# Performance work log

Hardware: AMD Instinct MI355X
Metric: run time of the kernel (lower is better)

The kernel has to match this reference:

```python
import jax, jax.numpy as jnp
import numpy as np

NP, NA = 200000, 100000        # paper / author node counts
EW, EC = 300000, 300000        # writes / cites edge counts
HID, H, D = 128, 4, 32         # hidden, heads, head dim
FIN_P, FIN_A, OUT = 256, 128, 16
SCALE = float(1.0 / np.sqrt(D))


def _seg_softmax(alpha, idx, n):
    # softmax over edges grouped by destination node (PyG softmax)
    m = jax.ops.segment_max(alpha, idx, num_segments=n)
    e = jnp.exp(alpha - m[idx])
    s = jax.ops.segment_sum(e, idx, num_segments=n)
    return e / (s[idx] + 1e-16)


def _edge_type(k_src, v_src, q_dst, src, dst, a_rel, m_rel, p_rel, n_dst):
    # per-relation transform at node level, then gather-attend-scatter
    kr = jnp.einsum('nhd,hde->nhe', k_src, a_rel)
    vr = jnp.einsum('nhd,hde->nhe', v_src, m_rel)
    alpha = jnp.sum(q_dst[dst] * kr[src], axis=-1) * p_rel * SCALE  # [E,H]
    alpha = _seg_softmax(alpha, dst, n_dst)
    return jax.ops.segment_sum(vr[src] * alpha[..., None], dst, num_segments=n_dst)


def setup_inputs() -> dict:
    key = jax.random.key(0)
    ks = iter(jax.random.split(key, 48))

    def nrm(shape, s=0.05):
        return jax.random.normal(next(ks), shape, jnp.float32) * s

    inp = dict(
        x_paper=nrm((NP, FIN_P), 1.0),
        x_author=nrm((NA, FIN_A), 1.0),
        writes_src=jax.random.randint(next(ks), (EW,), 0, NA, dtype=jnp.int32),
        writes_dst=jax.random.randint(next(ks), (EW,), 0, NP, dtype=jnp.int32),
        cites_src=jax.random.randint(next(ks), (EC,), 0, NP, dtype=jnp.int32),
        cites_dst=jax.random.randint(next(ks), (EC,), 0, NP, dtype=jnp.int32),
        lin_paper_w=nrm((FIN_P, HID)), lin_paper_b=jnp.zeros((HID,), jnp.float32),
        lin_author_w=nrm((FIN_A, HID)), lin_author_b=jnp.zeros((HID,), jnp.float32),
        lin_out_w=nrm((HID, OUT)), lin_out_b=jnp.zeros((OUT,), jnp.float32),
    )
    for t in ('paper', 'author'):
        for nm in ('k', 'q', 'v', 'a'):
            inp[f'{nm}_w_{t}'] = nrm((HID, HID))
            inp[f'{nm}_b_{t}'] = jnp.zeros((HID,), jnp.float32)
        inp[f'skip_{t}'] = jnp.ones((), jnp.float32)
    for e in ('writes', 'cites'):
        inp[f'a_rel_{e}'] = nrm((H, D, D), 0.18)
        inp[f'm_rel_{e}'] = nrm((H, D, D), 0.18)
        inp[f'p_rel_{e}'] = jnp.ones((H,), jnp.float32)
    return inp


def reference(x_paper, x_author, writes_src, writes_dst, cites_src, cites_dst,
              lin_paper_w, lin_paper_b, lin_author_w, lin_author_b,
              lin_out_w, lin_out_b,
              k_w_paper, k_b_paper, q_w_paper, q_b_paper, v_w_paper, v_b_paper,
              a_w_paper, a_b_paper, skip_paper,
              k_w_author, k_b_author, q_w_author, q_b_author, v_w_author, v_b_author,
              a_w_author, a_b_author, skip_author,
              a_rel_writes, m_rel_writes, p_rel_writes,
              a_rel_cites, m_rel_cites, p_rel_cites):
    # per-node-type input projection + relu
    hp = jax.nn.relu(x_paper @ lin_paper_w + lin_paper_b)
    ha = jax.nn.relu(x_author @ lin_author_w + lin_author_b)
    # HGTConv: per-node-type k/q/v, [N,H,D]
    k_p = (hp @ k_w_paper + k_b_paper).reshape(NP, H, D)
    q_p = (hp @ q_w_paper + q_b_paper).reshape(NP, H, D)
    v_p = (hp @ v_w_paper + v_b_paper).reshape(NP, H, D)
    k_a = (ha @ k_w_author + k_b_author).reshape(NA, H, D)
    v_a = (ha @ v_w_author + v_b_author).reshape(NA, H, D)
    # heterogeneous multi-relation attention, group='sum' over edge types
    out_p = _edge_type(k_a, v_a, q_p, writes_src, writes_dst,
                       a_rel_writes, m_rel_writes, p_rel_writes, NP)
    out_p = out_p + _edge_type(k_p, v_p, q_p, cites_src, cites_dst,
                               a_rel_cites, m_rel_cites, p_rel_cites, NP)
    # output projection + gated skip (paper type; only 'paper' feeds the head)
    op = jax.nn.gelu(out_p.reshape(NP, HID), approximate=False) @ a_w_paper + a_b_paper
    beta = jax.nn.sigmoid(skip_paper)
    hp = beta * op + (1.0 - beta) * hp
    return hp @ lin_out_w + lin_out_b  # [NP, OUT]
```

## Files before the change

kernel.cpp:

```cpp
#include <hip/hip_runtime.h>
#include <cstdint>

#define NP 200000
#define NA 100000
#define EW 300000
#define EC 300000
#define HID 128
#define FIN_P 256
#define FIN_A 128
#define NOUT 16
#define ATT_SCALE 0.17677669529663687f

#define NBP 1563
#define NBA 782

#define SCAN_N (2 * NP)
#define SCAN_BS 256
#define SCAN_ITEMS 4
#define SCAN_TILE 1024
#define SCAN_NB ((SCAN_N + SCAN_TILE - 1) / SCAN_TILE)

typedef short s8v __attribute__((ext_vector_type(8)));
typedef float f32x4 __attribute__((ext_vector_type(4)));
typedef unsigned short ushort_t;

__device__ __forceinline__ float gelu_f(float x) {
  return 0.5f * x * (1.0f + erff(x * 0.70710678118654752f));
}
__device__ __forceinline__ ushort_t f2bf(float f) {
  unsigned u = __float_as_uint(f);
  return (ushort_t)((u + 0x7FFFu + ((u >> 16) & 1u)) >> 16);
}
__device__ __forceinline__ unsigned pack2bf(float a, float b) {
  return (unsigned)f2bf(a) | ((unsigned)f2bf(b) << 16);
}
__device__ __forceinline__ unsigned cvtpk(float a, float b) {
  unsigned r;
  asm("v_cvt_pk_bf16_f32 %0, %1, %2" : "=v"(r) : "v"(a), "v"(b));
  return r;
}
__device__ __forceinline__ float bflo(unsigned u) { return __uint_as_float(u << 16); }
__device__ __forceinline__ float bfhi(unsigned u) { return __uint_as_float(u & 0xFFFF0000u); }

__device__ __forceinline__ void gl16(const void* g, void* l) {
  __builtin_amdgcn_global_load_lds(
      (const __attribute__((address_space(1))) void*)g,
      (__attribute__((address_space(3))) void*)l, 16, 0, 0);
}

__device__ __forceinline__ int s2row(int r) { return (r ^ (r >> 2)) & 3; }

__global__ void prep_all(
    const float* __restrict__ qw,  const float* __restrict__ qb,
    const float* __restrict__ kwp, const float* __restrict__ kbp, const float* __restrict__ arc,
    const float* __restrict__ vwp, const float* __restrict__ vbp, const float* __restrict__ mrc,
    const float* __restrict__ kwa, const float* __restrict__ kba, const float* __restrict__ arw,
    const float* __restrict__ vwa, const float* __restrict__ vba, const float* __restrict__ mrw,
    const float* __restrict__ lpw, const float* __restrict__ law,
    const float* __restrict__ aw, const float* __restrict__ ab,
    const float* __restrict__ skip, const float* __restrict__ W2, const float* __restrict__ b2,
    ushort_t* __restrict__ Wall, float* __restrict__ Ball,
    float* __restrict__ Wg, float* __restrict__ Wh, float* __restrict__ bo,
    int* __restrict__ cnt)
{
  const int b = blockIdx.x, tid = threadIdx.x;
  if (b == 0) {
    for (int idx = tid; idx < 16384; idx += 256) {
      int c = idx >> 7, r = idx & 127;
      Wall[idx] = f2bf(qw[r * 128 + c]);
    }
    for (int c = tid; c < 128; c += 256) Ball[c] = qb[c];
  } else if (b <= 4) {
    const float *W, *bias, *rel;
    switch (b) {
      case 1:  W = kwp; bias = kbp; rel = arc; break;
      case 2:  W = vwp; bias = vbp; rel = mrc; break;
      case 3:  W = kwa; bias = kba; rel = arw; break;
      default: W = vwa; bias = vba; rel = mrw; break;
    }
    for (int idx = tid; idx < 16384; idx += 256) {
      int c = idx >> 7, r = idx & 127, h = c >> 5, e = c & 31;
      float s = 0.f;
      #pragma unroll
      for (int d = 0; d < 32; ++d) s += W[r * 128 + h * 32 + d] * rel[h * 1024 + d * 32 + e];
      Wall[b * 16384 + idx] = f2bf(s);
    }
    for (int c = tid; c < 128; c += 256) {
      int h = c >> 5, e = c & 31;
      float s = 0.f;
      #pragma unroll
      for (int d = 0; d < 32; ++d) s += bias[h * 32 + d] * rel[h * 1024 + d * 32 + e];
      Ball[b * 128 + c] = s;
    }
  } else if (b == 5) {
    for (int idx = tid; idx < 16384; idx += 256) {
      int c = idx >> 7, r = idx & 127;
      Wall[5 * 16384 + idx] = f2bf(law[r * 128 + c]);
    }
  } else if (b == 6) {
    for (int idx = tid; idx < 32768; idx += 256) {
      int c = idx >> 8, r = idx & 255;
      Wall[6 * 16384 + idx] = f2bf(lpw[r * 128 + c]);
    }
  } else if (b == 7) {
    float beta = 1.0f / (1.0f + expf(-skip[0]));
    for (int idx = tid; idx < 128 * 16; idx += 256) {
      int r = idx >> 4, c = idx & 15;
      float s = 0.f;
      for (int k = 0; k < 128; ++k) s += aw[r * 128 + k] * W2[k * 16 + c];
      Wg[idx] = beta * s;
      Wh[idx] = (1.0f - beta) * W2[idx];
    }
    if (tid < 16) {
      float s = 0.f;
      for (int k = 0; k < 128; ++k) s += ab[k] * W2[k * 16 + tid];
      bo[tid] = beta * s + b2[tid];
    }
  } else {
    int chunk = SCAN_N / 8;
    int base = (b - 8) * chunk;
    for (int i = tid; i < chunk; i += 256) cnt[base + i] = 0;
  }
}

__global__ __launch_bounds__(256) void gemm_proj(
    const float* __restrict__ xp, const float* __restrict__ xa,
    const ushort_t* __restrict__ Wall,
    const float* __restrict__ bp, const float* __restrict__ ba,
    ushort_t* __restrict__ hpo, ushort_t* __restrict__ hao)
{
  __shared__ ushort_t As[4096];
  __shared__ ushort_t Bs[4096];
  const bool isP = blockIdx.x < NBP;
  const int bid = isP ? blockIdx.x : blockIdx.x - NBP;
  const float* A = isP ? xp : xa;
  const ushort_t* W = Wall + (isP ? 6 * 16384 : 5 * 16384);
  const float* bias = isP ? bp : ba;
  ushort_t* C = isP ? hpo : hao;
  const int M = isP ? NP : NA;
  const int KT = isP ? 256 : 128;
  const int nt = KT >> 5;

  const int tid  = threadIdx.x;
  const int lane = tid & 63;
  const int wv   = tid >> 6;
  const int wr   = wv >> 1, wc = wv & 1;
  const int l15  = lane & 15, kgl = lane >> 4;
  const int s2l  = (l15 ^ (l15 >> 2)) & 3;
  const int row0 = bid * 128;

  const int r0 = tid >> 2, kgp = tid & 3;
  const int sk = kgp ^ s2row(r0);
  int g0 = row0 + r0;       if (g0 > M - 1) g0 = M - 1;
  int g1 = row0 + r0 + 64;  if (g1 > M - 1) g1 = M - 1;
  const float* a0p = A + (size_t)g0 * KT + sk * 8;
  const float* a1p = A + (size_t)g1 * KT + sk * 8;
  const ushort_t* b0p = W + (size_t)r0 * KT + sk * 8;
  const ushort_t* b1p = W + (size_t)(r0 + 64) * KT + sk * 8;
  ushort_t* asd0 = &As[(size_t)tid * 8];
  ushort_t* asd1 = &As[(size_t)(tid + 256) * 8];

  f32x4 acc[4][4];
  #pragma unroll
  for (int i = 0; i < 4; ++i)
    #pragma unroll
    for (int j = 0; j < 4; ++j) acc[i][j] = (f32x4){0.f, 0.f, 0.f, 0.f};

  for (int kt = 0; kt < KT; kt += 32) {
    gl16(b0p + kt, &Bs[(size_t)tid * 8]);
    gl16(b1p + kt, &Bs[(size_t)(tid + 256) * 8]);
    float4 fa0 = *(const float4*)(a0p + kt);
    float4 fa1 = *(const float4*)(a0p + kt + 4);
    float4 fa2 = *(const float4*)(a1p + kt);
    float4 fa3 = *(const float4*)(a1p + kt + 4);
    uint4 v0, v1;
    v0.x = cvtpk(fa0.x, fa0.y); v0.y = cvtpk(fa0.z, fa0.w);
    v0.z = cvtpk(fa1.x, fa1.y); v0.w = cvtpk(fa1.z, fa1.w);
    v1.x = cvtpk(fa2.x, fa2.y); v1.y = cvtpk(fa2.z, fa2.w);
    v1.z = cvtpk(fa3.x, fa3.y); v1.w = cvtpk(fa3.z, fa3.w);
    *(uint4*)asd0 = v0;
    *(uint4*)asd1 = v1;
    __syncthreads();

    const s8v* As8 = (const s8v*)As;
    const s8v* Bs8 = (const s8v*)Bs;
    s8v af[4], bfv[4];
    #pragma unroll
    for (int i = 0; i < 4; ++i)
      af[i]  = As8[(wr * 64 + i * 16 + l15) * 4 + (kgl ^ s2l)];
    #pragma unroll
    for (int j = 0; j < 4; ++j)
      bfv[j] = Bs8[(wc * 64 + j * 16 + l15) * 4 + (kgl ^ s2l)];
    #pragma unroll
    for (int i = 0; i < 4; ++i)
      #pragma unroll
      for (int j = 0; j < 4; ++j)
        acc[i][j] = __builtin_amdgcn_mfma_f32_16x16x32_bf16(af[i], bfv[j], acc[i][j], 0, 0, 0);
    __syncthreads();
  }

  float bv[4];
  #pragma unroll
  for (int j = 0; j < 4; ++j) bv[j] = bias[wc * 64 + j * 16 + l15];
  #pragma unroll
  for (int i = 0; i < 4; ++i) {
    #pragma unroll
    for (int r = 0; r < 4; ++r) {
      int row = row0 + wr * 64 + i * 16 + kgl * 4 + r;
      if (row < M) {
        #pragma unroll
        for (int j = 0; j < 4; ++j) {
          float v = acc[i][j][r] + bv[j];
          v = fmaxf(v, 0.f);
          C[(size_t)row * 128 + wc * 64 + j * 16 + l15] = f2bf(v);
        }
      }
    }
  }
}

__global__ __launch_bounds__(256) void gemm_kv(
    const ushort_t* __restrict__ hpA, const ushort_t* __restrict__ haA,
    const ushort_t* __restrict__ Wall, const float* __restrict__ Ball,
    ushort_t* __restrict__ qkv, ushort_t* __restrict__ kvw)
{
  __shared__ ushort_t As[4096];
  __shared__ ushort_t Bs[4096];
  int b = blockIdx.x;
  int set, bid, M;
  const ushort_t* A;
  ushort_t* C;
  if (b < 3 * NBP) {
    set = b / NBP; bid = b - set * NBP;
    A = hpA; M = NP;
    C = qkv + (size_t)set * NP * HID;
  } else {
    int t = b - 3 * NBP;
    int s2 = t / NBA; bid = t - s2 * NBA;
    set = 3 + s2;
    A = haA; M = NA;
    C = kvw + (size_t)s2 * NA * HID;
  }
  const ushort_t* W = Wall + set * 16384;
  const float* bias = Ball + set * 128;

  const int tid  = threadIdx.x;
  const int lane = tid & 63;
  const int wv   = tid >> 6;
  const int wr   = wv >> 1, wc = wv & 1;
  const int l15  = lane & 15, kgl = lane >> 4;
  const int s2l  = (l15 ^ (l15 >> 2)) & 3;
  const int row0 = bid * 128;

  const int r0 = tid >> 2, kgp = tid & 3;
  const int sk = kgp ^ s2row(r0);
  int g0 = row0 + r0;       if (g0 > M - 1) g0 = M - 1;
  int g1 = row0 + r0 + 64;  if (g1 > M - 1) g1 = M - 1;
  const ushort_t* a0p = A + (size_t)g0 * 128 + sk * 8;
  const ushort_t* a1p = A + (size_t)g1 * 128 + sk * 8;
  const ushort_t* b0p = W + (size_t)r0 * 128 + sk * 8;
  const ushort_t* b1p = W + (size_t)(r0 + 64) * 128 + sk * 8;

  f32x4 acc[4][4];
  #pragma unroll
  for (int i = 0; i < 4; ++i)
    #pragma unroll
    for (int j = 0; j < 4; ++j) acc[i][j] = (f32x4){0.f, 0.f, 0.f, 0.f};

  #pragma unroll
  for (int t = 0; t < 4; ++t) {
    int kt = t * 32;
    gl16(a0p + kt, &As[(size_t)tid * 8]);
    gl16(a1p + kt, &As[(size_t)(tid + 256) * 8]);
    gl16(b0p + kt, &Bs[(size_t)tid * 8]);
    gl16(b1p + kt, &Bs[(size_t)(tid + 256) * 8]);
    __syncthreads();

    const s8v* As8 = (const s8v*)As;
    const s8v* Bs8 = (const s8v*)Bs;
    s8v af[4], bfv[4];
    #pragma unroll
    for (int i = 0; i < 4; ++i)
      af[i]  = As8[(wr * 64 + i * 16 + l15) * 4 + (kgl ^ s2l)];
    #pragma unroll
    for (int j = 0; j < 4; ++j)
      bfv[j] = Bs8[(wc * 64 + j * 16 + l15) * 4 + (kgl ^ s2l)];
    #pragma unroll
    for (int i = 0; i < 4; ++i)
      #pragma unroll
      for (int j = 0; j < 4; ++j)
        acc[i][j] = __builtin_amdgcn_mfma_f32_16x16x32_bf16(af[i], bfv[j], acc[i][j], 0, 0, 0);
    __syncthreads();
  }

  float bv[4];
  #pragma unroll
  for (int j = 0; j < 4; ++j) bv[j] = bias[wc * 64 + j * 16 + l15];
  #pragma unroll
  for (int i = 0; i < 4; ++i) {
    #pragma unroll
    for (int r = 0; r < 4; ++r) {
      int row = row0 + wr * 64 + i * 16 + kgl * 4 + r;
      if (row < M) {
        #pragma unroll
        for (int j = 0; j < 4; ++j) {
          C[(size_t)row * 128 + wc * 64 + j * 16 + l15] = f2bf(acc[i][j][r] + bv[j]);
        }
      }
    }
  }
}

__global__ void hist_k(const int* __restrict__ wdst, const int* __restrict__ cdst,
                       int* __restrict__ cnt)
{
  int t = blockIdx.x * blockDim.x + threadIdx.x;
  if (t < EW) atomicAdd(&cnt[wdst[t]], 1);
  if (t < EC) atomicAdd(&cnt[NP + cdst[t]], 1);
}

__global__ __launch_bounds__(SCAN_BS) void scan1(const int* __restrict__ cnt,
                                                 int* __restrict__ off,
                                                 int* __restrict__ bsum)
{
  __shared__ int sh[2][SCAN_BS];
  int tid = threadIdx.x;
  int base = blockIdx.x * SCAN_TILE + tid * SCAN_ITEMS;
  int v[SCAN_ITEMS]; int tsum = 0;
  #pragma unroll
  for (int i = 0; i < SCAN_ITEMS; ++i) {
    int idx = base + i;
    v[i] = (idx < SCAN_N) ? cnt[idx] : 0;
    tsum += v[i];
  }
  int p = 0;
  sh[0][tid] = tsum; __syncthreads();
  #pragma unroll
  for (int d = 1; d < SCAN_BS; d <<= 1) {
    int x = sh[p][tid] + ((tid >= d) ? sh[p][tid - d] : 0);
    sh[p ^ 1][tid] = x; __syncthreads(); p ^= 1;
  }
  int run = sh[p][tid] - tsum;
  #pragma unroll
  for (int i = 0; i < SCAN_ITEMS; ++i) {
    int idx = base + i;
    if (idx < SCAN_N) off[idx] = run;
    run += v[i];
  }
  if (tid == SCAN_BS - 1) bsum[blockIdx.x] = sh[p][tid];
}

__global__ __launch_bounds__(512) void scan2(int* __restrict__ bsum)
{
  __shared__ int sh[2][512];
  int tid = threadIdx.x;
  int v = (tid < SCAN_NB) ? bsum[tid] : 0;
  int p = 0;
  sh[0][tid] = v; __syncthreads();
  for (int d = 1; d < 512; d <<= 1) {
    int x = sh[p][tid] + ((tid >= d) ? sh[p][tid - d] : 0);
    sh[p ^ 1][tid] = x; __syncthreads(); p ^= 1;
  }
  if (tid < SCAN_NB) bsum[tid] = sh[p][tid] - v;
}

__global__ __launch_bounds__(SCAN_BS) void scan3(int* __restrict__ off, int* __restrict__ cur,
                                                 const int* __restrict__ bsum)
{
  int add = bsum[blockIdx.x];
  int base = blockIdx.x * SCAN_TILE + threadIdx.x;
  #pragma unroll
  for (int i = 0; i < SCAN_ITEMS; ++i) {
    int idx = base + i * SCAN_BS;
    if (idx < SCAN_N) { int t = off[idx] + add; off[idx] = t; cur[idx] = t; }
  }
  if (blockIdx.x == 0 && threadIdx.x == 0) off[SCAN_N] = EW + EC;
}

__global__ void fill_k(const int* __restrict__ wsrc, const int* __restrict__ wdst,
                       const int* __restrict__ csrc, const int* __restrict__ cdst,
                       int* __restrict__ cur, int* __restrict__ esrc)
{
  int t = blockIdx.x * blockDim.x + threadIdx.x;
  if (t < EW) { int p = atomicAdd(&cur[wdst[t]], 1); esrc[p] = wsrc[t] << 8; }
  if (t < EC) { int p = atomicAdd(&cur[NP + cdst[t]], 1); esrc[p] = csrc[t] << 8; }
}

__global__ __launch_bounds__(256) void node_attn(
    const int* __restrict__ off, const int* __restrict__ esrc,
    const ushort_t* __restrict__ q,
    const ushort_t* __restrict__ kr_w, const ushort_t* __restrict__ vr_w,
    const ushort_t* __restrict__ kr_c, const ushort_t* __restrict__ vr_c,
    const float* __restrict__ p_rel_w, const float* __restrict__ p_rel_c,
    ushort_t* __restrict__ out_p)
{
  int gid = blockIdx.x * blockDim.x + threadIdx.x;
  int node = gid >> 4;
  int l16 = gid & 15;
  int h = l16 >> 2;

  uint4 qv = *(const uint4*)(q + (size_t)node * HID + l16 * 8);
  float qf[8];
  {
    const unsigned* pq = (const unsigned*)&qv;
    #pragma unroll
    for (int w = 0; w < 4; ++w) { qf[2 * w] = bflo(pq[w]); qf[2 * w + 1] = bfhi(pq[w]); }
  }
  float prw = p_rel_w[h] * ATT_SCALE;
  float prc = p_rel_c[h] * ATT_SCALE;
  unsigned loff = (unsigned)(l16 * 16);

  float t[8];
  #pragma unroll
  for (int i = 0; i < 8; ++i) t[i] = 0.f;

  #pragma unroll
  for (int r = 0; r < 2; ++r) {
    const char* krb = (const char*)((r == 0) ? kr_w : kr_c);
    const char* vrb = (const char*)((r == 0) ? vr_w : vr_c);
    float prr = (r == 0) ? prw : prc;
    int eb = off[(r == 0 ? 0 : NP) + node];
    int ee = off[(r == 0 ? 0 : NP) + node + 1];

    float s = 0.f;
    float A[8];
    #pragma unroll
    for (int i = 0; i < 8; ++i) A[i] = 0.f;

    for (int e = eb; e < ee; ++e) {
      unsigned kb = (unsigned)esrc[e] + loff;
      uint4 kv = *(const uint4*)(krb + kb);
      uint4 vv = *(const uint4*)(vrb + kb);
      const unsigned* pk = (const unsigned*)&kv;
      float d = 0.f;
      #pragma unroll
      for (int w = 0; w < 4; ++w) {
        d = fmaf(qf[2 * w], bflo(pk[w]), d);
        d = fmaf(qf[2 * w + 1], bfhi(pk[w]), d);
      }
      d += __shfl_xor(d, 1);
      d += __shfl_xor(d, 2);
      float p = __expf(d * prr);
      s += p;
      const unsigned* pv = (const unsigned*)&vv;
      #pragma unroll
      for (int w = 0; w < 4; ++w) {
        A[2 * w]     = fmaf(p, bflo(pv[w]), A[2 * w]);
        A[2 * w + 1] = fmaf(p, bfhi(pv[w]), A[2 * w + 1]);
      }
    }
    float inv = 1.0f / (s + 1e-16f);
    #pragma unroll
    for (int i = 0; i < 8; ++i) t[i] = fmaf(A[i], inv, t[i]);
  }

  uint4 o;
  unsigned* po = (unsigned*)&o;
  #pragma unroll
  for (int w = 0; w < 4; ++w) po[w] = pack2bf(t[2 * w], t[2 * w + 1]);
  *(uint4*)(out_p + (size_t)node * HID + l16 * 8) = o;
}

__global__ __launch_bounds__(256) void epilogue_k(
    const ushort_t* __restrict__ out_p, const ushort_t* __restrict__ hp,
    const float* __restrict__ Wg, const float* __restrict__ Wh,
    const float* __restrict__ bo, float* __restrict__ out)
{
  __shared__ float Ts[64][129];
  __shared__ float Wgs[128][16];
  __shared__ float Whs[128][16];
  __shared__ float bs[16];
  int tid = threadIdx.x;
  int row0 = blockIdx.x * 64;

  #pragma unroll
  for (int i = 0; i < 2; ++i) {
    int idx = tid + i * 256;
    *(float4*)&Wgs[idx >> 2][(idx & 3) << 2] = *(const float4*)(Wg + (size_t)idx * 4);
    *(float4*)&Whs[idx >> 2][(idx & 3) << 2] = *(const float4*)(Wh + (size_t)idx * 4);
  }
  if (tid < 16) bs[tid] = bo[tid];

  #pragma unroll
  for (int i = 0; i < 4; ++i) {
    int idx = tid + i * 256;
    int r = idx >> 4, c8 = (idx & 15) << 3;
    uint4 g = *(const uint4*)(out_p + (size_t)(row0 + r) * HID + c8);
    const unsigned* pw = (const unsigned*)&g;
    #pragma unroll
    for (int w = 0; w < 4; ++w) {
      Ts[r][c8 + 2 * w]     = gelu_f(bflo(pw[w]));
      Ts[r][c8 + 2 * w + 1] = gelu_f(bfhi(pw[w]));
    }
  }
  __syncthreads();

  int row = tid & 63, cg = tid >> 6;
  float acc[4];
  #pragma unroll
  for (int j = 0; j < 4; ++j) acc[j] = bs[cg * 4 + j];
  for (int k = 0; k < 128; ++k) {
    float g = Ts[row][k];
    float4 w = *(const float4*)&Wgs[k][cg << 2];
    acc[0] = fmaf(g, w.x, acc[0]); acc[1] = fmaf(g, w.y, acc[1]);
    acc[2] = fmaf(g, w.z, acc[2]); acc[3] = fmaf(g, w.w, acc[3]);
  }
  __syncthreads();

  #pragma unroll
  for (int i = 0; i < 4; ++i) {
    int idx = tid + i * 256;
    int r = idx >> 4, c8 = (idx & 15) << 3;
    uint4 hh = *(const uint4*)(hp + (size_t)(row0 + r) * HID + c8);
    const unsigned* pw = (const unsigned*)&hh;
    #pragma unroll
    for (int w = 0; w < 4; ++w) {
      Ts[r][c8 + 2 * w]     = bflo(pw[w]);
      Ts[r][c8 + 2 * w + 1] = bfhi(pw[w]);
    }
  }
  __syncthreads();
  for (int k = 0; k < 128; ++k) {
    float hv = Ts[row][k];
    float4 w = *(const float4*)&Whs[k][cg << 2];
    acc[0] = fmaf(hv, w.x, acc[0]); acc[1] = fmaf(hv, w.y, acc[1]);
    acc[2] = fmaf(hv, w.z, acc[2]); acc[3] = fmaf(hv, w.w, acc[3]);
  }
  *(float4*)(out + (size_t)(row0 + row) * NOUT + (cg << 2)) =
      make_float4(acc[0], acc[1], acc[2], acc[3]);
}

extern "C" void kernel_launch(void* const* d_in, const int* in_sizes, int n_in,
                              void* d_out, int out_size, void* d_ws, size_t ws_size,
                              hipStream_t stream)
{
  (void)in_sizes; (void)n_in; (void)out_size; (void)ws_size;
  const float* x_paper      = (const float*)d_in[0];
  const float* x_author     = (const float*)d_in[1];
  const int*   writes_src   = (const int*)d_in[2];
  const int*   writes_dst   = (const int*)d_in[3];
  const int*   cites_src    = (const int*)d_in[4];
  const int*   cites_dst    = (const int*)d_in[5];
  const float* lin_paper_w  = (const float*)d_in[6];
  const float* lin_paper_b  = (const float*)d_in[7];
  const float* lin_author_w = (const float*)d_in[8];
  const float* lin_author_b = (const float*)d_in[9];
  const float* lin_out_w    = (const float*)d_in[10];
  const float* lin_out_b    = (const float*)d_in[11];
  const float* k_w_paper    = (const float*)d_in[12];
  const float* k_b_paper    = (const float*)d_in[13];
  const float* q_w_paper    = (const float*)d_in[14];
  const float* q_b_paper    = (const float*)d_in[15];
  const float* v_w_paper    = (const float*)d_in[16];
  const float* v_b_paper    = (const float*)d_in[17];
  const float* a_w_paper    = (const float*)d_in[18];
  const float* a_b_paper    = (const float*)d_in[19];
  const float* skip_paper   = (const float*)d_in[20];
  const float* k_w_author   = (const float*)d_in[21];
  const float* k_b_author   = (const float*)d_in[22];
  const float* v_w_author   = (const float*)d_in[25];
  const float* v_b_author   = (const float*)d_in[26];
  const float* a_rel_writes = (const float*)d_in[30];
  const float* m_rel_writes = (const float*)d_in[31];
  const float* p_rel_writes = (const float*)d_in[32];
  const float* a_rel_cites  = (const float*)d_in[33];
  const float* m_rel_cites  = (const float*)d_in[34];
  const float* p_rel_cites  = (const float*)d_in[35];

  float* ws = (float*)d_ws;
  size_t off_f = 0;
  auto nxt = [&](size_t nfloats) { float* p = ws + off_f; off_f += nfloats; return p; };
  ushort_t* hp    = (ushort_t*)nxt((size_t)NP * 64);
  ushort_t* ha    = (ushort_t*)nxt((size_t)NA * 64);
  ushort_t* qkv   = (ushort_t*)nxt((size_t)3 * NP * 64);
  ushort_t* kvw   = (ushort_t*)nxt((size_t)2 * NA * 64);
  ushort_t* outp  = (ushort_t*)nxt((size_t)NP * 64);
  int*      cnt   = (int*)nxt(SCAN_N);
  int*      offs  = (int*)nxt(SCAN_N + 2);
  int*      cur   = (int*)nxt(SCAN_N);
  int*      esrc  = (int*)nxt(EW + EC);
  int*      bsum  = (int*)nxt(512);
  ushort_t* Wall  = (ushort_t*)nxt(65536);
  float*    Ball  = nxt(5 * 128);
  float*    Wg    = nxt(2048);
  float*    Wh    = nxt(2048);
  float*    bo    = nxt(16);

  ushort_t* q_p  = qkv;
  ushort_t* kr_c = qkv + (size_t)NP * HID;
  ushort_t* vr_c = qkv + (size_t)2 * NP * HID;
  ushort_t* kr_w = kvw;
  ushort_t* vr_w = kvw + (size_t)NA * HID;

  prep_all<<<16, 256, 0, stream>>>(q_w_paper, q_b_paper,
                                   k_w_paper, k_b_paper, a_rel_cites,
                                   v_w_paper, v_b_paper, m_rel_cites,
                                   k_w_author, k_b_author, a_rel_writes,
                                   v_w_author, v_b_author, m_rel_writes,
                                   lin_paper_w, lin_author_w,
                                   a_w_paper, a_b_paper, skip_paper, lin_out_w, lin_out_b,
                                   Wall, Ball, Wg, Wh, bo, cnt);

  hist_k<<<(300000 + 255) / 256, 256, 0, stream>>>(writes_dst, cites_dst, cnt);
  scan1<<<SCAN_NB, SCAN_BS, 0, stream>>>(cnt, offs, bsum);
  scan2<<<1, 512, 0, stream>>>(bsum);
  scan3<<<SCAN_NB, SCAN_BS, 0, stream>>>(offs, cur, bsum);
  fill_k<<<(300000 + 255) / 256, 256, 0, stream>>>(writes_src, writes_dst,
                                                   cites_src, cites_dst, cur, esrc);

  gemm_proj<<<NBP + NBA, 256, 0, stream>>>(x_paper, x_author, Wall,
                                           lin_paper_b, lin_author_b, hp, ha);
  gemm_kv<<<3 * NBP + 2 * NBA, 256, 0, stream>>>(hp, ha, Wall, Ball, qkv, kvw);

  node_attn<<<(NP * 16) / 256, 256, 0, stream>>>(
      offs, esrc, q_p, kr_w, vr_w, kr_c, vr_c, p_rel_writes, p_rel_cites, outp);

  epilogue_k<<<(NP + 63) / 64, 256, 0, stream>>>(outp, hp, Wg, Wh, bo, (float*)d_out);
}
```

Before: 439.7 us.

## Reuse A tile across all weight sets in gemm_kv and prefetch first edges in attention

New measurement: 425.3 us. 3.3% less time.

```diff
diff --git a/kernel.cpp b/kernel.cpp
--- a/kernel.cpp
+++ b/kernel.cpp
@@ -139,7 +139,6 @@
   ushort_t* C = isP ? hpo : hao;
   const int M = isP ? NP : NA;
   const int KT = isP ? 256 : 128;
-  const int nt = KT >> 5;
 
   const int tid  = threadIdx.x;
   const int lane = tid & 63;
@@ -224,25 +223,14 @@
     const ushort_t* __restrict__ Wall, const float* __restrict__ Ball,
     ushort_t* __restrict__ qkv, ushort_t* __restrict__ kvw)
 {
-  __shared__ ushort_t As[4096];
-  __shared__ ushort_t Bs[4096];
-  int b = blockIdx.x;
-  int set, bid, M;
-  const ushort_t* A;
-  ushort_t* C;
-  if (b < 3 * NBP) {
-    set = b / NBP; bid = b - set * NBP;
-    A = hpA; M = NP;
-    C = qkv + (size_t)set * NP * HID;
-  } else {
-    int t = b - 3 * NBP;
-    int s2 = t / NBA; bid = t - s2 * NBA;
-    set = 3 + s2;
-    A = haA; M = NA;
-    C = kvw + (size_t)s2 * NA * HID;
-  }
-  const ushort_t* W = Wall + set * 16384;
-  const float* bias = Ball + set * 128;
+  __shared__ ushort_t As[16384];
+  __shared__ ushort_t Bs[16384];
+  const bool isP = blockIdx.x < NBP;
+  const int bid = isP ? blockIdx.x : blockIdx.x - NBP;
+  const ushort_t* A = isP ? hpA : haA;
+  const int M = isP ? NP : NA;
+  const int base_set = isP ? 0 : 3;
+  const int nsets = isP ? 3 : 2;
 
   const int tid  = threadIdx.x;
   const int lane = tid & 63;
@@ -258,56 +246,69 @@
   int g1 = row0 + r0 + 64;  if (g1 > M - 1) g1 = M - 1;
   const ushort_t* a0p = A + (size_t)g0 * 128 + sk * 8;
   const ushort_t* a1p = A + (size_t)g1 * 128 + sk * 8;
-  const ushort_t* b0p = W + (size_t)r0 * 128 + sk * 8;
-  const ushort_t* b1p = W + (size_t)(r0 + 64) * 128 + sk * 8;
-
-  f32x4 acc[4][4];
-  #pragma unroll
-  for (int i = 0; i < 4; ++i)
-    #pragma unroll
-    for (int j = 0; j < 4; ++j) acc[i][j] = (f32x4){0.f, 0.f, 0.f, 0.f};
 
   #pragma unroll
   for (int t = 0; t < 4; ++t) {
-    int kt = t * 32;
-    gl16(a0p + kt, &As[(size_t)tid * 8]);
-    gl16(a1p + kt, &As[(size_t)(tid + 256) * 8]);
-    gl16(b0p + kt, &Bs[(size_t)tid * 8]);
-    gl16(b1p + kt, &Bs[(size_t)(tid + 256) * 8]);
+    gl16(a0p + t * 32, &As[((size_t)t * 512 + tid) * 8]);
+    gl16(a1p + t * 32, &As[((size_t)t * 512 + tid + 256) * 8]);
+  }
+
+  for (int si = 0; si < nsets; ++si) {
+    const int set = base_set + si;
+    const ushort_t* W = Wall + set * 16384;
+    const float* bias = Ball + set * 128;
+    ushort_t* C = isP ? (qkv + (size_t)set * NP * HID)
+                      : (kvw + (size_t)(set - 3) * NA * HID);
+    const ushort_t* b0p = W + (size_t)r0 * 128 + sk * 8;
+    const ushort_t* b1p = W + (size_t)(r0 + 64) * 128 + sk * 8;
+    #pragma unroll
+    for (int t = 0; t < 4; ++t) {
+      gl16(b0p + t * 32, &Bs[((size_t)t * 512 + tid) * 8]);
+      gl16(b1p + t * 32, &Bs[((size_t)t * 512 + tid + 256) * 8]);
+    }
     __syncthreads();
+
+    f32x4 acc[4][4];
+    #pragma unroll
+    for (int i = 0; i < 4; ++i)
+      #pragma unroll
+      for (int j = 0; j < 4; ++j) acc[i][j] = (f32x4){0.f, 0.f, 0.f, 0.f};
 
     const s8v* As8 = (const s8v*)As;
     const s8v* Bs8 = (const s8v*)Bs;
-    s8v af[4], bfv[4];
-    #pragma unroll
-    for (int i = 0; i < 4; ++i)
-      af[i]  = As8[(wr * 64 + i * 16 + l15) * 4 + (kgl ^ s2l)];
-    #pragma unroll
-    for (int j = 0; j < 4; ++j)
-      bfv[j] = Bs8[(wc * 64 + j * 16 + l15) * 4 + (kgl ^ s2l)];
-    #pragma unroll
-    for (int i = 0; i < 4; ++i)
+    #pragma unroll
+    for (int t = 0; t < 4; ++t) {
+      s8v af[4], bfv[4];
+      #pragma unroll
+      for (int i = 0; i < 4; ++i)
+        af[i]  = As8[t * 512 + (wr * 64 + i * 16 + l15) * 4 + (kgl ^ s2l)];
       #pragma unroll
       for (int j = 0; j < 4; ++j)
-        acc[i][j] = __builtin_amdgcn_mfma_f32_16x16x32_bf16(af[i], bfv[j], acc[i][j], 0, 0, 0);
-    __syncthreads();
-  }
-
-  float bv[4];
-  #pragma unroll
-  for (int j = 0; j < 4; ++j) bv[j] = bias[wc * 64 + j * 16 + l15];
-  #pragma unroll
-  for (int i = 0; i < 4; ++i) {
-    #pragma unroll
-    for (int r = 0; r < 4; ++r) {
-      int row = row0 + wr * 64 + i * 16 + kgl * 4 + r;
-      if (row < M) {
+        bfv[j] = Bs8[t * 512 + (wc * 64 + j * 16 + l15) * 4 + (kgl ^ s2l)];
+      #pragma unroll
+      for (int i = 0; i < 4; ++i)
         #pragma unroll
-        for (int j = 0; j < 4; ++j) {
-          C[(size_t)row * 128 + wc * 64 + j * 16 + l15] = f2bf(acc[i][j][r] + bv[j]);
+        for (int j = 0; j < 4; ++j)
+          acc[i][j] = __builtin_amdgcn_mfma_f32_16x16x32_bf16(af[i], bfv[j], acc[i][j], 0, 0, 0);
+    }
+
+    float bv[4];
+    #pragma unroll
+    for (int j = 0; j < 4; ++j) bv[j] = bias[wc * 64 + j * 16 + l15];
+    #pragma unroll
+    for (int i = 0; i < 4; ++i) {
+      #pragma unroll
+      for (int r = 0; r < 4; ++r) {
+        int row = row0 + wr * 64 + i * 16 + kgl * 4 + r;
+        if (row < M) {
+          #pragma unroll
+          for (int j = 0; j < 4; ++j) {
+            C[(size_t)row * 128 + wc * 64 + j * 16 + l15] = f2bf(acc[i][j][r] + bv[j]);
+          }
         }
       }
     }
+    __syncthreads();
   }
 }
 
@@ -398,8 +399,23 @@
   int node = gid >> 4;
   int l16 = gid & 15;
   int h = l16 >> 2;
+  unsigned loff = (unsigned)(l16 * 16);
+
+  int eb0 = off[node],      ee0 = off[node + 1];
+  int eb1 = off[NP + node], ee1 = off[NP + node + 1];
 
   uint4 qv = *(const uint4*)(q + (size_t)node * HID + l16 * 8);
+
+  int pi0 = (eb0 < ee0) ? eb0 : 0;
+  int pi1 = (eb1 < ee1) ? eb1 : 0;
+  unsigned pb0 = (unsigned)esrc[pi0] + loff;
+  unsigned pb1 = (unsigned)esrc[pi1] + loff;
+  uint4 pk[2], pv[2];
+  pk[0] = *(const uint4*)((const char*)kr_w + pb0);
+  pv[0] = *(const uint4*)((const char*)vr_w + pb0);
+  pk[1] = *(const uint4*)((const char*)kr_c + pb1);
+  pv[1] = *(const uint4*)((const char*)vr_c + pb1);
+
   float qf[8];
   {
     const unsigned* pq = (const unsigned*)&qv;
@@ -408,7 +424,6 @@
   }
   float prw = p_rel_w[h] * ATT_SCALE;
   float prc = p_rel_c[h] * ATT_SCALE;
-  unsigned loff = (unsigned)(l16 * 16);
 
   float t[8];
   #pragma unroll
@@ -419,34 +434,55 @@
     const char* krb = (const char*)((r == 0) ? kr_w : kr_c);
     const char* vrb = (const char*)((r == 0) ? vr_w : vr_c);
     float prr = (r == 0) ? prw : prc;
-    int eb = off[(r == 0 ? 0 : NP) + node];
-    int ee = off[(r == 0 ? 0 : NP) + node + 1];
+    int eb = (r == 0) ? eb0 : eb1;
+    int ee = (r == 0) ? ee0 : ee1;
 
     float s = 0.f;
     float A[8];
     #pragma unroll
     for (int i = 0; i < 8; ++i) A[i] = 0.f;
 
-    for (int e = eb; e < ee; ++e) {
-      unsigned kb = (unsigned)esrc[e] + loff;
-      uint4 kv = *(const uint4*)(krb + kb);
-      uint4 vv = *(const uint4*)(vrb + kb);
-      const unsigned* pk = (const unsigned*)&kv;
+    int e = eb;
+    if (e < ee) {
+      const unsigned* k8 = (const unsigned*)&pk[r];
+      const unsigned* v8 = (const unsigned*)&pv[r];
       float d = 0.f;
       #pragma unroll
       for (int w = 0; w < 4; ++w) {
-        d = fmaf(qf[2 * w], bflo(pk[w]), d);
-        d = fmaf(qf[2 * w + 1], bfhi(pk[w]), d);
+        d = fmaf(qf[2 * w], bflo(k8[w]), d);
+        d = fmaf(qf[2 * w + 1], bfhi(k8[w]), d);
       }
       d += __shfl_xor(d, 1);
       d += __shfl_xor(d, 2);
       float p = __expf(d * prr);
       s += p;
-      const unsigned* pv = (const unsigned*)&vv;
       #pragma unroll
       for (int w = 0; w < 4; ++w) {
-        A[2 * w]     = fmaf(p, bflo(pv[w]), A[2 * w]);
-        A[2 * w + 1] = fmaf(p, bfhi(pv[w]), A[2 * w + 1]);
+        A[2 * w]     = fmaf(p, bflo(v8[w]), A[2 * w]);
+        A[2 * w + 1] = fmaf(p, bfhi(v8[w]), A[2 * w + 1]);
+      }
+      ++e;
+    }
+    for (; e < ee; ++e) {
+      unsigned kb = (unsigned)esrc[e] + loff;
+      uint4 kv = *(const uint4*)(krb + kb);
+      uint4 vv = *(const uint4*)(vrb + kb);
+      const unsigned* k8 = (const unsigned*)&kv;
+      float d = 0.f;
+      #pragma unroll
+      for (int w = 0; w < 4; ++w) {
+        d = fmaf(qf[2 * w], bflo(k8[w]), d);
+        d = fmaf(qf[2 * w + 1], bfhi(k8[w]), d);
+      }
+      d += __shfl_xor(d, 1);
+      d += __shfl_xor(d, 2);
+      float p = __expf(d * prr);
+      s += p;
+      const unsigned* v8 = (const unsigned*)&vv;
+      #pragma unroll
+      for (int w = 0; w < 4; ++w) {
+        A[2 * w]     = fmaf(p, bflo(v8[w]), A[2 * w]);
+        A[2 * w + 1] = fmaf(p, bfhi(v8[w]), A[2 * w + 1]);
       }
     }
     float inv = 1.0f / (s + 1e-16f);
@@ -610,7 +646,7 @@
 
   gemm_proj<<<NBP + NBA, 256, 0, stream>>>(x_paper, x_author, Wall,
                                            lin_paper_b, lin_author_b, hp, ha);
-  gemm_kv<<<3 * NBP + 2 * NBA, 256, 0, stream>>>(hp, ha, Wall, Ball, qkv, kvw);
+  gemm_kv<<<NBP + NBA, 256, 0, stream>>>(hp, ha, Wall, Ball, qkv, kvw);
 
   node_attn<<<(NP * 16) / 256, 256, 0, stream>>>(
       offs, esrc, q_p, kr_w, vr_w, kr_c, vr_c, p_rel_writes, p_rel_cites, outp);
```
